# Performance work log

Measured on AMD Instinct MI355X. Metric: run time of the kernel, lower is better.

Reference implementation:

```python
import jax, jax.numpy as jnp
import numpy as np

B, S, H = 1, 2048, 1024
NH, NKV, HD = 16, 4, 64  # n_attn_heads, n_kv_heads, head_dim


def setup_inputs() -> dict:
    key = jax.random.key(0)
    k1, k2, k3, k4 = jax.random.split(key, 4)
    x = jax.random.normal(k1, (B, S, H), dtype=jnp.float32)
    Wq = jax.random.normal(k2, (H, H), dtype=jnp.float32) * 0.02
    Wk = jax.random.normal(k3, (NKV * HD, H), dtype=jnp.float32) * 0.02
    Wv = jax.random.normal(k4, (NKV * HD, H), dtype=jnp.float32) * 0.02
    return {"x": x, "Wq": Wq, "Wk": Wk, "Wv": Wv}


def reference(x, Wq, Wk, Wv):
    b, s, h = x.shape
    rep = NH // NKV
    # projections (torch Linear: x @ W.T)
    q = (x @ Wq.T).reshape(b, s, NH, HD).transpose(0, 2, 1, 3)      # [b, NH, s, d]
    k = (x @ Wk.T).reshape(b, s, NKV, HD).transpose(0, 2, 1, 3)     # [b, NKV, s, d]
    v = (x @ Wv.T).reshape(b, s, NKV, HD).transpose(0, 2, 1, 3)
    # repeat_kv: expand each kv head rep times
    k = jnp.repeat(k, rep, axis=1)                                   # [b, NH, s, d]
    v = jnp.repeat(v, rep, axis=1)
    # NOTE: source scales by 1/sqrt(hidden_size), not 1/sqrt(head_dim)
    scale = 1.0 / np.sqrt(H).astype(np.float32)
    scores = jnp.einsum('bhqd,bhkd->bhqk', q, k) * scale             # [b, NH, s, s]
    causal = jnp.tril(jnp.ones((s, s), dtype=bool))
    scores = jnp.where(causal[None, None], scores, -jnp.inf)
    probs = jax.nn.softmax(scores, axis=-1)
    y = jnp.einsum('bhqk,bhkd->bhqd', probs, v)                      # [b, NH, s, d]
    return y.transpose(0, 2, 1, 3).reshape(b, s, NH * HD)
```

## Files before the change

### kernel.cpp

```cpp
#include <hip/hip_runtime.h>

#define S_LEN 2048
#define HID   1024
#define NHEAD 16
#define NKVH  4
#define HDIM  64
#define NPROJ 1536
#define QKSTR 1280

typedef __bf16 bf16x8 __attribute__((ext_vector_type(8)));
typedef __bf16 bf16x4 __attribute__((ext_vector_type(4)));
typedef __bf16 bf16x2 __attribute__((ext_vector_type(2)));
typedef float  f32x4  __attribute__((ext_vector_type(4)));
typedef unsigned u32x4 __attribute__((ext_vector_type(4)));

typedef const __attribute__((address_space(1))) void* gas_ptr;
typedef __attribute__((address_space(3))) void*       las_ptr;

#define QSCALE 0.04508422f

__device__ __forceinline__ unsigned short f2bf(float f) {
    unsigned u = __builtin_bit_cast(unsigned, f);
    u = u + 0x7FFFu + ((u >> 16) & 1u);
    return (unsigned short)(u >> 16);
}

__global__ __launch_bounds__(256) void cvt_all(
    const float* __restrict__ x,  const float* __restrict__ wq,
    const float* __restrict__ wk, const float* __restrict__ wv,
    unsigned short* __restrict__ xbf, unsigned short* __restrict__ wbf)
{
    const long nx  = (long)S_LEN * HID;
    const long nwq = (long)HID * HID;
    const long nwk = (long)256 * HID;
    long i = (long)(blockIdx.x * 256 + threadIdx.x) * 4;
    const float* src; unsigned short* dst;
    if (i < nx)                  { src = x  + i;                 dst = xbf + i; }
    else if (i < nx + nwq)       { long j = i - nx;              src = wq + j; dst = wbf + j; }
    else if (i < nx + nwq + nwk) { long j = i - nx - nwq;        src = wk + j; dst = wbf + nwq + j; }
    else                         { long j = i - nx - nwq - nwk;  src = wv + j; dst = wbf + nwq + nwk + j; }
    float4 v = *(const float4*)src;
    ushort4 o; o.x = f2bf(v.x); o.y = f2bf(v.y); o.z = f2bf(v.z); o.w = f2bf(v.w);
    *(ushort4*)dst = o;
}

__global__ __launch_bounds__(256, 2) void proj_gemm(
    const unsigned short* __restrict__ xbf,
    const unsigned short* __restrict__ wbf,
    unsigned short* __restrict__ qkv,
    unsigned short* __restrict__ vT)
{
    __shared__ unsigned short At[2][64 * 64];
    __shared__ unsigned short Bt[2][96 * 64];
    const int tid = threadIdx.x;
    const int w = tid >> 6, l = tid & 63;
    const int quad = l >> 4, lane16 = l & 15;
    const int m0 = blockIdx.y * 64, n0 = blockIdx.x * 96;
    const int wm = (w & 1) * 32, wn = (w >> 1) * 48;

    const int srow = l >> 3;
    const int scol = ((l & 7) ^ srow) * 8;

    f32x4 acc[2][3] = {};

    #define STAGE(KT, BUF)                                                              \
        do {                                                                            \
            _Pragma("unroll")                                                           \
            for (int c = 0; c < 2; ++c) {                                               \
                const int rbase = w * 16 + c * 8;                                       \
                const unsigned short* ga =                                              \
                    xbf + (long)(m0 + rbase + srow) * HID + (KT) + scol;                \
                __builtin_amdgcn_global_load_lds((gas_ptr)ga,                           \
                    (las_ptr)&At[BUF][rbase * 64], 16, 0, 0);                           \
            }                                                                           \
            _Pragma("unroll")                                                           \
            for (int c = 0; c < 3; ++c) {                                               \
                const int rbase = w * 24 + c * 8;                                       \
                const unsigned short* gb =                                              \
                    wbf + (long)(n0 + rbase + srow) * HID + (KT) + scol;                \
                __builtin_amdgcn_global_load_lds((gas_ptr)gb,                           \
                    (las_ptr)&Bt[BUF][rbase * 64], 16, 0, 0);                           \
            }                                                                           \
        } while (0)

    STAGE(0, 0);

    for (int i = 0; i < 16; ++i) {
        const int cur = i & 1;
        __syncthreads();
        if (i + 1 < 16) STAGE((i + 1) * 64, cur ^ 1);

        #pragma unroll
        for (int ks = 0; ks < 2; ++ks) {
            const int swz = ((ks * 4 + quad) ^ (lane16 & 7)) * 8;
            bf16x8 a[2], b[3];
            #pragma unroll
            for (int mi = 0; mi < 2; ++mi)
                a[mi] = *(const bf16x8*)&At[cur][(wm + mi * 16 + lane16) * 64 + swz];
            #pragma unroll
            for (int ni = 0; ni < 3; ++ni)
                b[ni] = *(const bf16x8*)&Bt[cur][(wn + ni * 16 + lane16) * 64 + swz];
            #pragma unroll
            for (int mi = 0; mi < 2; ++mi)
                #pragma unroll
                for (int ni = 0; ni < 3; ++ni)
                    acc[mi][ni] = __builtin_amdgcn_mfma_f32_16x16x32_bf16(a[mi], b[ni], acc[mi][ni], 0, 0, 0);
        }
    }
    #undef STAGE

    #pragma unroll
    for (int mi = 0; mi < 2; ++mi) {
        const int row = m0 + wm + mi * 16 + quad * 4;
        #pragma unroll
        for (int ni = 0; ni < 3; ++ni) {
            const int col = n0 + wn + ni * 16 + lane16;
            #pragma unroll
            for (int r = 0; r < 4; ++r) {
                const float v = acc[mi][ni][r];
                if (col < 1024)
                    qkv[(long)(row + r) * QKSTR + col] = f2bf(v * QSCALE);
                else if (col < 1280)
                    qkv[(long)(row + r) * QKSTR + col] = f2bf(v);
                else
                    vT[(long)(col - 1280) * S_LEN + (row + r)] = f2bf(v);
            }
        }
    }
}

#define KSTR 72
__global__ __launch_bounds__(256, 3) void attn(
    const unsigned short* __restrict__ qkv,
    const unsigned short* __restrict__ vT,
    float* __restrict__ out)
{
    __shared__ unsigned short Kt[2][64 * KSTR];
    __shared__ unsigned short Vt[2][64 * KSTR];

    const int tid = threadIdx.x;
    const int w = tid >> 6, l = tid & 63;
    const int quad = l >> 4, lane16 = l & 15;
    const int bx = blockIdx.x, by = blockIdx.y;
    const int qt = (by & 8) ? (31 - bx) : bx;
    const int h  = by;
    const int kh = h >> 2;
    const int qcol = h * 64;
    const int kcol = 1024 + kh * 64;

    const long qrow = (long)(qt * 64 + w * 16 + lane16);
    bf16x8 qa0 = *(const bf16x8*)&qkv[qrow * QKSTR + qcol + quad * 8];
    bf16x8 qa1 = *(const bf16x8*)&qkv[qrow * QKSTR + qcol + 32 + quad * 8];

    f32x4 o[4] = {};
    float rsum[4] = {0.f, 0.f, 0.f, 0.f};

    const int sr = tid >> 2, ss = tid & 3;
    const long vrow = (long)(kh * 64 + sr) * S_LEN;

    const int srcA = lane16 + ((l & 16) << 1);
    const int srcB = srcA + 16;
    const bool up = (l >= 32);

    bf16x8 kr0, kr1, vr0, vr1;
    {
        const long gk = (long)sr * QKSTR + kcol + ss * 16;
        kr0 = *(const bf16x8*)&qkv[gk];
        kr1 = *(const bf16x8*)&qkv[gk + 8];
        const long gv = vrow + ss * 16;
        vr0 = *(const bf16x8*)&vT[gv];
        vr1 = *(const bf16x8*)&vT[gv + 8];
    }

    for (int kt = 0; kt <= qt; ++kt) {
        const int cur = kt & 1;
        *(bf16x8*)&Kt[cur][sr * KSTR + ss * 16]     = kr0;
        *(bf16x8*)&Kt[cur][sr * KSTR + ss * 16 + 8] = kr1;
        *(bf16x8*)&Vt[cur][sr * KSTR + ss * 16]     = vr0;
        *(bf16x8*)&Vt[cur][sr * KSTR + ss * 16 + 8] = vr1;
        if (kt < qt) {
            const long gk = (long)((kt + 1) * 64 + sr) * QKSTR + kcol + ss * 16;
            kr0 = *(const bf16x8*)&qkv[gk];
            kr1 = *(const bf16x8*)&qkv[gk + 8];
            const long gv = vrow + (kt + 1) * 64 + ss * 16;
            vr0 = *(const bf16x8*)&vT[gv];
            vr1 = *(const bf16x8*)&vT[gv + 8];
        }
        __syncthreads();

        f32x4 sacc[4] = {};
        __builtin_amdgcn_s_setprio(1);
        #pragma unroll
        for (int t = 0; t < 4; ++t) {
            bf16x8 kb0 = *(const bf16x8*)&Kt[cur][(t * 16 + lane16) * KSTR + quad * 8];
            bf16x8 kb1 = *(const bf16x8*)&Kt[cur][(t * 16 + lane16) * KSTR + 32 + quad * 8];
            sacc[t] = __builtin_amdgcn_mfma_f32_16x16x32_bf16(kb0, qa0, sacc[t], 0, 0, 0);
            sacc[t] = __builtin_amdgcn_mfma_f32_16x16x32_bf16(kb1, qa1, sacc[t], 0, 0, 0);
        }
        __builtin_amdgcn_s_setprio(0);

        if (kt == qt) {
            #pragma unroll
            for (int t = 0; t < 4; ++t) {
                const int kvw = t * 16 + quad * 4;
                #pragma unroll
                for (int r = 0; r < 4; ++r)
                    if (kvw + r > w * 16 + lane16) sacc[t][r] = -3.0e38f;
            }
        }

        unsigned h8[8];
        #pragma unroll
        for (int t = 0; t < 4; ++t) {
            const float p0 = __builtin_amdgcn_exp2f(sacc[t][0]);
            const float p1 = __builtin_amdgcn_exp2f(sacc[t][1]);
            const float p2 = __builtin_amdgcn_exp2f(sacc[t][2]);
            const float p3 = __builtin_amdgcn_exp2f(sacc[t][3]);
            rsum[t] += (p0 + p1) + (p2 + p3);
            bf16x2 lo, hi;
            lo[0] = (__bf16)p0; lo[1] = (__bf16)p1;
            hi[0] = (__bf16)p2; hi[1] = (__bf16)p3;
            h8[t * 2]     = __builtin_bit_cast(unsigned, lo);
            h8[t * 2 + 1] = __builtin_bit_cast(unsigned, hi);
        }

        unsigned sA[8], sB[8];
        #pragma unroll
        for (int i = 0; i < 8; ++i) {
            sA[i] = __shfl(h8[i], srcA);
            sB[i] = __shfl(h8[i], srcB);
        }
        u32x4 w0, w1;
        w0[0] = up ? sA[2] : sA[0];  w0[1] = up ? sA[3] : sA[1];
        w0[2] = up ? sB[2] : sB[0];  w0[3] = up ? sB[3] : sB[1];
        w1[0] = up ? sA[6] : sA[4];  w1[1] = up ? sA[7] : sA[5];
        w1[2] = up ? sB[6] : sB[4];  w1[3] = up ? sB[7] : sB[5];
        const bf16x8 pa0 = __builtin_bit_cast(bf16x8, w0);
        const bf16x8 pa1 = __builtin_bit_cast(bf16x8, w1);

        __builtin_amdgcn_s_setprio(1);
        #pragma unroll
        for (int t = 0; t < 4; ++t) {
            bf16x8 vb0 = *(const bf16x8*)&Vt[cur][(t * 16 + lane16) * KSTR + quad * 8];
            o[t] = __builtin_amdgcn_mfma_f32_16x16x32_bf16(pa0, vb0, o[t], 0, 0, 0);
        }
        #pragma unroll
        for (int t = 0; t < 4; ++t) {
            bf16x8 vb1 = *(const bf16x8*)&Vt[cur][(t * 16 + lane16) * KSTR + 32 + quad * 8];
            o[t] = __builtin_amdgcn_mfma_f32_16x16x32_bf16(pa1, vb1, o[t], 0, 0, 0);
        }
        __builtin_amdgcn_s_setprio(0);
    }

    float total = (rsum[0] + rsum[1]) + (rsum[2] + rsum[3]);
    total += __shfl_xor(total, 16);
    total += __shfl_xor(total, 32);
    const float invt = 1.0f / total;
    float inv[4];
    #pragma unroll
    for (int r = 0; r < 4; ++r)
        inv[r] = __shfl(invt, quad * 4 + r);

    const int orow = qt * 64 + w * 16 + quad * 4;
    #pragma unroll
    for (int t = 0; t < 4; ++t) {
        const int col = h * 64 + t * 16 + lane16;
        #pragma unroll
        for (int r = 0; r < 4; ++r)
            out[(long)(orow + r) * (NHEAD * HDIM) + col] = o[t][r] * inv[r];
    }
}

extern "C" void kernel_launch(void* const* d_in, const int* in_sizes, int n_in,
                              void* d_out, int out_size, void* d_ws, size_t ws_size,
                              hipStream_t stream) {
    const float* x  = (const float*)d_in[0];
    const float* wq = (const float*)d_in[1];
    const float* wk = (const float*)d_in[2];
    const float* wv = (const float*)d_in[3];
    float* out = (float*)d_out;

    unsigned short* xbf = (unsigned short*)d_ws;
    unsigned short* wbf = xbf + (size_t)S_LEN * HID;
    unsigned short* qkv = wbf + (size_t)NPROJ * HID;
    unsigned short* vT  = qkv + (size_t)S_LEN * QKSTR;

    cvt_all<<<dim3(3584), dim3(256), 0, stream>>>(x, wq, wk, wv, xbf, wbf);
    proj_gemm<<<dim3(16, 32), dim3(256), 0, stream>>>(xbf, wbf, qkv, vT);
    attn<<<dim3(32, 16), dim3(256), 0, stream>>>(qkv, vT, out);
}
```

Measured before the change: 115.8 us.

## Give each attention warp two 16-row query tiles and halve the block size

The attention kernel now runs 2 warps per block instead of 4, and each warp handles 32 query rows as two 16-row m-tiles. Each K/V fragment loaded from shared memory is reused across both m-tiles, which halves LDS reads per MFMA. Each thread now loads twice as much of the K/V tile into LDS. The cost is more registers per thread and fewer warps per block for hiding latency; launch bounds change to (128,2).

```diff
diff --git a/kernel.cpp b/kernel.cpp
--- a/kernel.cpp
+++ b/kernel.cpp
@@ -130,7 +130,7 @@
 }
 
 #define KSTR 72
-__global__ __launch_bounds__(256, 3) void attn(
+__global__ __launch_bounds__(128, 2) void attn(
     const unsigned short* __restrict__ qkv,
     const unsigned short* __restrict__ vT,
     float* __restrict__ out)
@@ -148,126 +148,152 @@
     const int qcol = h * 64;
     const int kcol = 1024 + kh * 64;
 
-    const long qrow = (long)(qt * 64 + w * 16 + lane16);
-    bf16x8 qa0 = *(const bf16x8*)&qkv[qrow * QKSTR + qcol + quad * 8];
-    bf16x8 qa1 = *(const bf16x8*)&qkv[qrow * QKSTR + qcol + 32 + quad * 8];
-
-    f32x4 o[4] = {};
-    float rsum[4] = {0.f, 0.f, 0.f, 0.f};
-
-    const int sr = tid >> 2, ss = tid & 3;
+    bf16x8 qa[2][2];
+    #pragma unroll
+    for (int m = 0; m < 2; ++m) {
+        const long qrow = (long)(qt * 64 + w * 32 + m * 16 + lane16);
+        qa[m][0] = *(const bf16x8*)&qkv[qrow * QKSTR + qcol + quad * 8];
+        qa[m][1] = *(const bf16x8*)&qkv[qrow * QKSTR + qcol + 32 + quad * 8];
+    }
+
+    f32x4 o[2][4] = {};
+    float rsum[2][4] = {};
+
+    const int sr = tid >> 1, ss = tid & 1;
     const long vrow = (long)(kh * 64 + sr) * S_LEN;
 
     const int srcA = lane16 + ((l & 16) << 1);
     const int srcB = srcA + 16;
     const bool up = (l >= 32);
 
-    bf16x8 kr0, kr1, vr0, vr1;
+    bf16x8 kr[4], vr[4];
     {
-        const long gk = (long)sr * QKSTR + kcol + ss * 16;
-        kr0 = *(const bf16x8*)&qkv[gk];
-        kr1 = *(const bf16x8*)&qkv[gk + 8];
-        const long gv = vrow + ss * 16;
-        vr0 = *(const bf16x8*)&vT[gv];
-        vr1 = *(const bf16x8*)&vT[gv + 8];
+        const long gk = (long)sr * QKSTR + kcol + ss * 32;
+        const long gv = vrow + ss * 32;
+        #pragma unroll
+        for (int j = 0; j < 4; ++j) {
+            kr[j] = *(const bf16x8*)&qkv[gk + j * 8];
+            vr[j] = *(const bf16x8*)&vT[gv + j * 8];
+        }
     }
 
     for (int kt = 0; kt <= qt; ++kt) {
         const int cur = kt & 1;
-        *(bf16x8*)&Kt[cur][sr * KSTR + ss * 16]     = kr0;
-        *(bf16x8*)&Kt[cur][sr * KSTR + ss * 16 + 8] = kr1;
-        *(bf16x8*)&Vt[cur][sr * KSTR + ss * 16]     = vr0;
-        *(bf16x8*)&Vt[cur][sr * KSTR + ss * 16 + 8] = vr1;
+        #pragma unroll
+        for (int j = 0; j < 4; ++j) {
+            *(bf16x8*)&Kt[cur][sr * KSTR + ss * 32 + j * 8] = kr[j];
+            *(bf16x8*)&Vt[cur][sr * KSTR + ss * 32 + j * 8] = vr[j];
+        }
         if (kt < qt) {
-            const long gk = (long)((kt + 1) * 64 + sr) * QKSTR + kcol + ss * 16;
-            kr0 = *(const bf16x8*)&qkv[gk];
-            kr1 = *(const bf16x8*)&qkv[gk + 8];
-            const long gv = vrow + (kt + 1) * 64 + ss * 16;
-            vr0 = *(const bf16x8*)&vT[gv];
-            vr1 = *(const bf16x8*)&vT[gv + 8];
+            const long gk = (long)((kt + 1) * 64 + sr) * QKSTR + kcol + ss * 32;
+            const long gv = vrow + (kt + 1) * 64 + ss * 32;
+            #pragma unroll
+            for (int j = 0; j < 4; ++j) {
+                kr[j] = *(const bf16x8*)&qkv[gk + j * 8];
+                vr[j] = *(const bf16x8*)&vT[gv + j * 8];
+            }
         }
         __syncthreads();
 
-        f32x4 sacc[4] = {};
+        bf16x8 kb[8];
+        #pragma unroll
+        for (int t = 0; t < 4; ++t) {
+            kb[2 * t]     = *(const bf16x8*)&Kt[cur][(t * 16 + lane16) * KSTR + quad * 8];
+            kb[2 * t + 1] = *(const bf16x8*)&Kt[cur][(t * 16 + lane16) * KSTR + 32 + quad * 8];
+        }
+
+        f32x4 sacc[2][4] = {};
         __builtin_amdgcn_s_setprio(1);
         #pragma unroll
-        for (int t = 0; t < 4; ++t) {
-            bf16x8 kb0 = *(const bf16x8*)&Kt[cur][(t * 16 + lane16) * KSTR + quad * 8];
-            bf16x8 kb1 = *(const bf16x8*)&Kt[cur][(t * 16 + lane16) * KSTR + 32 + quad * 8];
-            sacc[t] = __builtin_amdgcn_mfma_f32_16x16x32_bf16(kb0, qa0, sacc[t], 0, 0, 0);
-            sacc[t] = __builtin_amdgcn_mfma_f32_16x16x32_bf16(kb1, qa1, sacc[t], 0, 0, 0);
-        }
+        for (int m = 0; m < 2; ++m)
+            #pragma unroll
+            for (int t = 0; t < 4; ++t) {
+                sacc[m][t] = __builtin_amdgcn_mfma_f32_16x16x32_bf16(kb[2 * t],     qa[m][0], sacc[m][t], 0, 0, 0);
+                sacc[m][t] = __builtin_amdgcn_mfma_f32_16x16x32_bf16(kb[2 * t + 1], qa[m][1], sacc[m][t], 0, 0, 0);
+            }
         __builtin_amdgcn_s_setprio(0);
 
         if (kt == qt) {
             #pragma unroll
+            for (int m = 0; m < 2; ++m) {
+                const int qloc = w * 32 + m * 16 + lane16;
+                #pragma unroll
+                for (int t = 0; t < 4; ++t) {
+                    const int kvw = t * 16 + quad * 4;
+                    #pragma unroll
+                    for (int r = 0; r < 4; ++r)
+                        if (kvw + r > qloc) sacc[m][t][r] = -3.0e38f;
+                }
+            }
+        }
+
+        bf16x8 pa[2][2];
+        #pragma unroll
+        for (int m = 0; m < 2; ++m) {
+            unsigned h8[8];
+            #pragma unroll
             for (int t = 0; t < 4; ++t) {
-                const int kvw = t * 16 + quad * 4;
-                #pragma unroll
-                for (int r = 0; r < 4; ++r)
-                    if (kvw + r > w * 16 + lane16) sacc[t][r] = -3.0e38f;
-            }
-        }
-
-        unsigned h8[8];
-        #pragma unroll
-        for (int t = 0; t < 4; ++t) {
-            const float p0 = __builtin_amdgcn_exp2f(sacc[t][0]);
-            const float p1 = __builtin_amdgcn_exp2f(sacc[t][1]);
-            const float p2 = __builtin_amdgcn_exp2f(sacc[t][2]);
-            const float p3 = __builtin_amdgcn_exp2f(sacc[t][3]);
-            rsum[t] += (p0 + p1) + (p2 + p3);
-            bf16x2 lo, hi;
-            lo[0] = (__bf16)p0; lo[1] = (__bf16)p1;
-            hi[0] = (__bf16)p2; hi[1] = (__bf16)p3;
-            h8[t * 2]     = __builtin_bit_cast(unsigned, lo);
-            h8[t * 2 + 1] = __builtin_bit_cast(unsigned, hi);
-        }
-
-        unsigned sA[8], sB[8];
-        #pragma unroll
-        for (int i = 0; i < 8; ++i) {
-            sA[i] = __shfl(h8[i], srcA);
-            sB[i] = __shfl(h8[i], srcB);
-        }
-        u32x4 w0, w1;
-        w0[0] = up ? sA[2] : sA[0];  w0[1] = up ? sA[3] : sA[1];
-        w0[2] = up ? sB[2] : sB[0];  w0[3] = up ? sB[3] : sB[1];
-        w1[0] = up ? sA[6] : sA[4];  w1[1] = up ? sA[7] : sA[5];
-        w1[2] = up ? sB[6] : sB[4];  w1[3] = up ? sB[7] : sB[5];
-        const bf16x8 pa0 = __builtin_bit_cast(bf16x8, w0);
-        const bf16x8 pa1 = __builtin_bit_cast(bf16x8, w1);
+                const float p0 = __builtin_amdgcn_exp2f(sacc[m][t][0]);
+                const float p1 = __builtin_amdgcn_exp2f(sacc[m][t][1]);
+                const float p2 = __builtin_amdgcn_exp2f(sacc[m][t][2]);
+                const float p3 = __builtin_amdgcn_exp2f(sacc[m][t][3]);
+                rsum[m][t] += (p0 + p1) + (p2 + p3);
+                bf16x2 lo, hi;
+                lo[0] = (__bf16)p0; lo[1] = (__bf16)p1;
+                hi[0] = (__bf16)p2; hi[1] = (__bf16)p3;
+                h8[t * 2]     = __builtin_bit_cast(unsigned, lo);
+                h8[t * 2 + 1] = __builtin_bit_cast(unsigned, hi);
+            }
+            unsigned sA[8], sB[8];
+            #pragma unroll
+            for (int i = 0; i < 8; ++i) {
+                sA[i] = __shfl(h8[i], srcA);
+                sB[i] = __shfl(h8[i], srcB);
+            }
+            u32x4 w0, w1;
+            w0[0] = up ? sA[2] : sA[0];  w0[1] = up ? sA[3] : sA[1];
+            w0[2] = up ? sB[2] : sB[0];  w0[3] = up ? sB[3] : sB[1];
+            w1[0] = up ? sA[6] : sA[4];  w1[1] = up ? sA[7] : sA[5];
+            w1[2] = up ? sB[6] : sB[4];  w1[3] = up ? sB[7] : sB[5];
+            pa[m][0] = __builtin_bit_cast(bf16x8, w0);
+            pa[m][1] = __builtin_bit_cast(bf16x8, w1);
+        }
 
         __builtin_amdgcn_s_setprio(1);
         #pragma unroll
         for (int t = 0; t < 4; ++t) {
             bf16x8 vb0 = *(const bf16x8*)&Vt[cur][(t * 16 + lane16) * KSTR + quad * 8];
-            o[t] = __builtin_amdgcn_mfma_f32_16x16x32_bf16(pa0, vb0, o[t], 0, 0, 0);
+            o[0][t] = __builtin_amdgcn_mfma_f32_16x16x32_bf16(pa[0][0], vb0, o[0][t], 0, 0, 0);
+            o[1][t] = __builtin_amdgcn_mfma_f32_16x16x32_bf16(pa[1][0], vb0, o[1][t], 0, 0, 0);
         }
         #pragma unroll
         for (int t = 0; t < 4; ++t) {
             bf16x8 vb1 = *(const bf16x8*)&Vt[cur][(t * 16 + lane16) * KSTR + 32 + quad * 8];
-            o[t] = __builtin_amdgcn_mfma_f32_16x16x32_bf16(pa1, vb1, o[t], 0, 0, 0);
+            o[0][t] = __builtin_amdgcn_mfma_f32_16x16x32_bf16(pa[0][1], vb1, o[0][t], 0, 0, 0);
+            o[1][t] = __builtin_amdgcn_mfma_f32_16x16x32_bf16(pa[1][1], vb1, o[1][t], 0, 0, 0);
         }
         __builtin_amdgcn_s_setprio(0);
     }
 
-    float total = (rsum[0] + rsum[1]) + (rsum[2] + rsum[3]);
-    total += __shfl_xor(total, 16);
-    total += __shfl_xor(total, 32);
-    const float invt = 1.0f / total;
-    float inv[4];
     #pragma unroll
-    for (int r = 0; r < 4; ++r)
-        inv[r] = __shfl(invt, quad * 4 + r);
-
-    const int orow = qt * 64 + w * 16 + quad * 4;
-    #pragma unroll
-    for (int t = 0; t < 4; ++t) {
-        const int col = h * 64 + t * 16 + lane16;
+    for (int m = 0; m < 2; ++m) {
+        float total = (rsum[m][0] + rsum[m][1]) + (rsum[m][2] + rsum[m][3]);
+        total += __shfl_xor(total, 16);
+        total += __shfl_xor(total, 32);
+        const float invt = 1.0f / total;
+        float inv[4];
         #pragma unroll
         for (int r = 0; r < 4; ++r)
-            out[(long)(orow + r) * (NHEAD * HDIM) + col] = o[t][r] * inv[r];
+            inv[r] = __shfl(invt, quad * 4 + r);
+
+        const int orow = qt * 64 + w * 32 + m * 16 + quad * 4;
+        #pragma unroll
+        for (int t = 0; t < 4; ++t) {
+            const int col = h * 64 + t * 16 + lane16;
+            #pragma unroll
+            for (int r = 0; r < 4; ++r)
+                out[(long)(orow + r) * (NHEAD * HDIM) + col] = o[m][t][r] * inv[r];
+        }
     }
 }
 
@@ -287,5 +313,5 @@
 
     cvt_all<<<dim3(3584), dim3(256), 0, stream>>>(x, wq, wk, wv, xbf, wbf);
     proj_gemm<<<dim3(16, 32), dim3(256), 0, stream>>>(xbf, wbf, qkv, vT);
-    attn<<<dim3(32, 16), dim3(256), 0, stream>>>(qkv, vT, out);
-}
+    attn<<<dim3(32, 16), dim3(128), 0, stream>>>(qkv, vT, out);
+}
```

Measured after the change: 121.5 us. 1.05x slower.
